# Kernel tuning notes

Hardware: AMD Instinct MI355X
Metric: run time of the kernel (lower is better)

Reference implementation:

```python
import jax, jax.numpy as jnp
import numpy as np

SLOPE = 0.2  # leaky_relu_slope for both LVC block and kernel predictor (passed through)
DILATIONS = (1, 3, 9, 27)
HOP = 256
STRIDE = 8
IN_CH = 32
KSZ = 3  # conv_kernel_size


def conv1d(x, w, b, dilation=1, padding=0):
    # x: (B,C,T), w: (O,I,K) torch layout
    y = jax.lax.conv_general_dilated(
        x, w, window_strides=(1,), padding=[(padding, padding)],
        rhs_dilation=(dilation,), dimension_numbers=('NCH', 'OIH', 'NCH'))
    return y + b[None, :, None]


def conv_transpose1d(x, w, b, stride, padding, output_padding=0):
    # w: torch ConvTranspose1d layout (Cin, Cout, K)
    w_ = jnp.flip(w, -1).transpose(1, 0, 2)  # (Cout, Cin, K)
    K = w.shape[2]
    pad = (K - 1 - padding, K - 1 - padding + output_padding)
    y = jax.lax.conv_general_dilated(
        x, w_, window_strides=(1,), padding=[pad],
        lhs_dilation=(stride,), dimension_numbers=('NCH', 'OIH', 'NCH'))
    return y + b[None, :, None]


def lrelu(x, slope=SLOPE):
    return jnp.where(x >= 0, x, slope * x)


def location_variable_convolution(x, kernel, bias, hop):
    # x: (B,C,T), kernel: (B,C,O,k,L), bias: (B,O,L); T == L*hop; dilation==1 path
    B, C, T = x.shape
    _, _, O, k, L = kernel.shape
    pad = (k - 1) // 2
    xp = jnp.pad(x, ((0, 0), (0, 0), (pad, pad)))
    # gather per-segment sliding windows: (L, hop, k) index into time axis
    idx = (jnp.arange(L)[:, None, None] * hop
           + jnp.arange(hop)[None, :, None]
           + jnp.arange(k)[None, None, :])
    xw = xp[:, :, idx]  # (B, C, L, hop, k)
    o = jnp.einsum('bclsk,bcokl->bols', xw, kernel)  # (B, O, L, hop)
    o = o + bias[:, :, :, None]
    return o.reshape(B, O, L * hop)


def kernel_predictor(spec, kp_in_w, kp_in_b, rb_w1, rb_b1, rb_w2, rb_b2,
                     kern_w, kern_b, bias_w, bias_b):
    B, _, L = spec.shape
    h = conv1d(spec, kp_in_w, kp_in_b, padding=2)  # k=5, pad=2
    for i in range(3):  # num_blocks = 3
        r = h
        h = conv1d(h, rb_w1[i], rb_b1[i], padding=1)
        h = lrelu(h)
        h = conv1d(h, rb_w2[i], rb_b2[i], padding=1)
        h = lrelu(h) + r
    kh = conv1d(h, kern_w, kern_b, padding=1)
    bh = conv1d(h, bias_w, bias_b, padding=1)
    n_layers = len(DILATIONS)
    kernels = kh.reshape(B, n_layers, IN_CH, 2 * IN_CH, KSZ, L)
    biases = bh.reshape(B, n_layers, 2 * IN_CH, L)
    return kernels, biases


def reference(hidden_states, spectrogram, convt_w, convt_b, kp_in_w, kp_in_b,
              rb_w1, rb_b1, rb_w2, rb_b2, kern_w, kern_b, bias_w, bias_b,
              lvc_w, lvc_b):
    h = conv_transpose1d(hidden_states, convt_w, convt_b,
                         stride=STRIDE, padding=STRIDE // 2 + STRIDE % 2,
                         output_padding=STRIDE % 2)
    kernels, biases = kernel_predictor(spectrogram, kp_in_w, kp_in_b,
                                       rb_w1, rb_b1, rb_w2, rb_b2,
                                       kern_w, kern_b, bias_w, bias_b)
    for i, d in enumerate(DILATIONS):
        r = h
        h = lrelu(h)
        h = conv1d(h, lvc_w[i], lvc_b[i], dilation=d, padding=d * (KSZ - 1) // 2)
        h = lrelu(h)
        h = location_variable_convolution(h, kernels[:, i], biases[:, i], HOP)
        h = jax.nn.sigmoid(h[:, :IN_CH, :]) * jnp.tanh(h[:, IN_CH:, :]) + r
    return h


def setup_inputs() -> dict:
    key = jax.random.key(0)
    ks = jax.random.split(key, 12)
    B, COND, L, H = 4, 100, 256, 64
    T = L * HOP  # 65536 output samples
    s = jnp.float32(0.02)
    d = {}
    d['hidden_states'] = jax.random.normal(ks[0], (B, IN_CH, T // STRIDE), jnp.float32)
    d['spectrogram'] = jax.random.normal(ks[1], (B, COND, L), jnp.float32)
    d['convt_w'] = jax.random.normal(ks[2], (IN_CH, IN_CH, 2 * STRIDE), jnp.float32) * s
    d['convt_b'] = jnp.zeros((IN_CH,), jnp.float32)
    d['kp_in_w'] = jax.random.normal(ks[3], (H, COND, 5), jnp.float32) * s
    d['kp_in_b'] = jnp.zeros((H,), jnp.float32)
    d['rb_w1'] = jax.random.normal(ks[4], (3, H, H, 3), jnp.float32) * s
    d['rb_b1'] = jnp.zeros((3, H), jnp.float32)
    d['rb_w2'] = jax.random.normal(ks[5], (3, H, H, 3), jnp.float32) * s
    d['rb_b2'] = jnp.zeros((3, H), jnp.float32)
    KC = IN_CH * 2 * IN_CH * KSZ * len(DILATIONS)  # 24576
    d['kern_w'] = jax.random.normal(ks[6], (KC, H, 3), jnp.float32) * s
    d['kern_b'] = jnp.zeros((KC,), jnp.float32)
    BC = 2 * IN_CH * len(DILATIONS)  # 256
    d['bias_w'] = jax.random.normal(ks[7], (BC, H, 3), jnp.float32) * s
    d['bias_b'] = jnp.zeros((BC,), jnp.float32)
    d['lvc_w'] = jax.random.normal(ks[8], (len(DILATIONS), IN_CH, IN_CH, 3), jnp.float32) * s
    d['lvc_b'] = jnp.zeros((len(DILATIONS), IN_CH), jnp.float32)
    return d
```

## Files before the change

kernel.cpp:

```cpp
#include <hip/hip_runtime.h>
#include <math.h>

#define NB 4
#define T 65536
#define TIN 8192
#define LL 256
#define KCL 6144

__device__ __forceinline__ float lrelu_f(float v) { return v >= 0.f ? v : 0.2f * v; }

__global__ void __launch_bounds__(256, 3) convt_kernel(const float* __restrict__ x,
                                                       const float* __restrict__ w,
                                                       const float* __restrict__ bias,
                                                       float* __restrict__ out) {
    const int bx = blockIdx.x, mt = blockIdx.y, b = blockIdx.z;
    const int tid = threadIdx.x;
    const int lane = tid & 63, wv = tid >> 6;
    const int s0base = bx * 256;
    __shared__ float xs[32][264];
    __shared__ float wm[64][64];

    const float* xb = x + (size_t)b * 32 * TIN;
    for (int idx = tid; idx < 32 * 64; idx += 256) {
        int c = idx >> 6, q = idx & 63;
        int p = s0base + q * 4;
        float4 v = (p + 3 < TIN) ? *(const float4*)(xb + c * TIN + p)
                                 : make_float4(0.f, 0.f, 0.f, 0.f);
        *(float4*)&xs[c][4 + 4 * q] = v;
    }
    if (tid < 32) {
        int p = s0base - 1;
        xs[tid][3] = (p >= 0) ? xb[tid * TIN + p] : 0.f;
    }
    for (int idx = tid; idx < 4096; idx += 256) {
        int i = idx >> 6, mm = idx & 63;
        int oo = mt * 8 + (mm >> 3), k0 = mm & 7;
        wm[i][mm] = (i < 32) ? w[i * 512 + oo * 16 + k0]
                             : w[(i - 32) * 512 + oo * 16 + k0 + 8];
    }
    __syncthreads();

    float acc[2][8][4];
#pragma unroll
    for (int ol = 0; ol < 2; ++ol) {
        float bo = bias[mt * 8 + wv * 2 + ol];
#pragma unroll
        for (int k0 = 0; k0 < 8; ++k0)
#pragma unroll
            for (int si = 0; si < 4; ++si) acc[ol][k0][si] = bo;
    }

    for (int c = 0; c < 32; ++c) {
        float xm1[4], x0[4];
#pragma unroll
        for (int si = 0; si < 4; ++si) {
            xm1[si] = xs[c][lane + si * 64 + 3];
            x0[si]  = xs[c][lane + si * 64 + 4];
        }
        float w0[16], w1[16];
#pragma unroll
        for (int q = 0; q < 4; ++q) {
            *(float4*)&w0[q * 4] = *(const float4*)&wm[c][wv * 16 + q * 4];
            *(float4*)&w1[q * 4] = *(const float4*)&wm[32 + c][wv * 16 + q * 4];
        }
#pragma unroll
        for (int ol = 0; ol < 2; ++ol)
#pragma unroll
            for (int k0 = 0; k0 < 8; ++k0)
#pragma unroll
                for (int si = 0; si < 4; ++si)
                    acc[ol][k0][si] += x0[si] * w0[ol * 8 + k0] + xm1[si] * w1[ol * 8 + k0];
    }

#pragma unroll
    for (int ol = 0; ol < 2; ++ol) {
        float* ob = out + ((size_t)b * 32 + mt * 8 + wv * 2 + ol) * T;
#pragma unroll
        for (int si = 0; si < 4; ++si) {
            int tb = (s0base + lane + si * 64) * 8 - 4;
            if (tb >= 0 && tb < T)
                *(float4*)(ob + tb) = make_float4(acc[ol][0][si], acc[ol][1][si],
                                                  acc[ol][2][si], acc[ol][3][si]);
            if (tb + 4 >= 0 && tb + 4 < T)
                *(float4*)(ob + tb + 4) = make_float4(acc[ol][4][si], acc[ol][5][si],
                                                      acc[ol][6][si], acc[ol][7][si]);
        }
    }
}

__global__ void __launch_bounds__(512) trunk_fused(
    const float* __restrict__ spec,
    const float* __restrict__ kp_in_w, const float* __restrict__ kp_in_b,
    const float* __restrict__ rb_w1, const float* __restrict__ rb_b1,
    const float* __restrict__ rb_w2, const float* __restrict__ rb_b2,
    const float* __restrict__ bias_w, const float* __restrict__ bias_b,
    float* __restrict__ kp_h, float* __restrict__ bh) {
    const int lq = blockIdx.x, b = blockIdx.y;
    const int tid = threadIdx.x;
    const int j = tid & 63;
    const int wvu = tid >> 6;
    const int oc0 = wvu * 8;
    const int l0 = lq * 32;
    const int labs = l0 - 9 + j;
    const bool lvalid = (labs >= 0 && labs < 256);

    __shared__ float hs[64][56];
    __shared__ float xsp[20][56];
    __shared__ float wt[192][68];

    float pw[24];
    float px[3];

    auto pf_kpin = [&](int cc) {
#pragma unroll
        for (int t = 0; t < 13; ++t) {
            int idx = t * 512 + tid;
            pw[t] = 0.f;
            if (idx < 6400) pw[t] = kp_in_w[(size_t)(idx / 100) * 500 + cc * 100 + (idx % 100)];
        }
    };
    auto wr_kpin = [&]() {
#pragma unroll
        for (int t = 0; t < 13; ++t) {
            int idx = t * 512 + tid;
            if (idx < 6400) wt[idx % 100][idx / 100] = pw[t];
        }
    };
    auto pf_xsp = [&](int cc) {
#pragma unroll
        for (int t = 0; t < 3; ++t) {
            int idx = t * 512 + tid;
            px[t] = 0.f;
            if (idx < 1120) {
                int c = idx / 56, jj = idx - c * 56;
                int l = l0 - 9 + jj;
                if (l >= 0 && l < 256)
                    px[t] = spec[((size_t)b * 100 + cc * 20 + c) * LL + l];
            }
        }
    };
    auto wr_xsp = [&]() {
#pragma unroll
        for (int t = 0; t < 3; ++t) {
            int idx = t * 512 + tid;
            if (idx < 1120) xsp[idx / 56][idx % 56] = px[t];
        }
    };
    auto pf_w192 = [&](const float* src) {
#pragma unroll
        for (int t = 0; t < 24; ++t) pw[t] = src[t * 512 + tid];
    };
    auto wr_w192 = [&]() {
#pragma unroll
        for (int t = 0; t < 24; ++t) {
            int idx = t * 512 + tid;
            wt[idx % 192][idx / 192] = pw[t];
        }
    };
    auto conv64 = [&](int jlo, int jhi, const float* bptr, float* a) {
#pragma unroll
        for (int oi = 0; oi < 8; ++oi) a[oi] = bptr[oc0 + oi];
        if (j >= jlo && j < jhi) {
            for (int c = 0; c < 64; ++c) {
                float x0 = hs[c][j - 1], x1 = hs[c][j], x2 = hs[c][j + 1];
#pragma unroll
                for (int k = 0; k < 3; ++k) {
                    float xk = (k == 0) ? x0 : (k == 1) ? x1 : x2;
                    float w8[8];
                    *(float4*)&w8[0] = *(const float4*)&wt[c * 3 + k][oc0];
                    *(float4*)&w8[4] = *(const float4*)&wt[c * 3 + k][oc0 + 4];
#pragma unroll
                    for (int oi = 0; oi < 8; ++oi) a[oi] += xk * w8[oi];
                }
            }
        }
    };

    pf_kpin(0); pf_xsp(0);
    wr_kpin(); wr_xsp();
    __syncthreads();

    float acc[8];
#pragma unroll
    for (int oi = 0; oi < 8; ++oi) acc[oi] = kp_in_b[oc0 + oi];

    for (int cc = 0; cc < 5; ++cc) {
        if (cc < 4) { pf_kpin(cc + 1); pf_xsp(cc + 1); }
        else        { pf_w192(rb_w1); }
        if (j >= 2 && j < 48) {
            for (int c = 0; c < 20; ++c) {
                float x5[5];
#pragma unroll
                for (int u = 0; u < 5; ++u) x5[u] = xsp[c][j - 2 + u];
#pragma unroll
                for (int k = 0; k < 5; ++k) {
                    float w8[8];
                    *(float4*)&w8[0] = *(const float4*)&wt[c * 5 + k][oc0];
                    *(float4*)&w8[4] = *(const float4*)&wt[c * 5 + k][oc0 + 4];
#pragma unroll
                    for (int oi = 0; oi < 8; ++oi) acc[oi] += x5[k] * w8[oi];
                }
            }
        }
        if (cc == 4 && j >= 2 && j < 48) {
#pragma unroll
            for (int oi = 0; oi < 8; ++oi) hs[oc0 + oi][j] = lvalid ? acc[oi] : 0.f;
        }
        __syncthreads();
        if (cc < 4) { wr_kpin(); wr_xsp(); }
        else        { wr_w192(); }
        __syncthreads();
    }

    for (int i = 0; i < 3; ++i) {
        const int jlo1 = 3 + 2 * i, jhi1 = 47 - 2 * i;
        const int jlo2 = jlo1 + 1, jhi2 = jhi1 - 1;
        float r[8];
        if (j >= jlo2 && j < jhi2) {
#pragma unroll
            for (int oi = 0; oi < 8; ++oi) r[oi] = hs[oc0 + oi][j];
        }
        pf_w192(rb_w2 + (size_t)i * 12288);
        float a1[8];
        conv64(jlo1, jhi1, rb_b1 + i * 64, a1);
        __syncthreads();
        if (j >= jlo1 && j < jhi1) {
#pragma unroll
            for (int oi = 0; oi < 8; ++oi) hs[oc0 + oi][j] = lvalid ? lrelu_f(a1[oi]) : 0.f;
        }
        wr_w192();
        __syncthreads();
        pf_w192(i < 2 ? rb_w1 + (size_t)(i + 1) * 12288 : bias_w);
        float a2[8];
        conv64(jlo2, jhi2, rb_b2 + i * 64, a2);
        __syncthreads();
        if (j >= jlo2 && j < jhi2) {
#pragma unroll
            for (int oi = 0; oi < 8; ++oi) hs[oc0 + oi][j] = lvalid ? (lrelu_f(a2[oi]) + r[oi]) : 0.f;
        }
        wr_w192();
        __syncthreads();
    }

    for (int idx = tid; idx < 64 * 32; idx += 512) {
        int c = idx >> 5, jj = idx & 31;
        kp_h[((size_t)b * 64 + c) * LL + l0 + jj] = hs[c][9 + jj];
    }

    for (int g = 0; g < 4; ++g) {
        if (g < 3) pf_w192(bias_w + (size_t)(g + 1) * 12288);
        float a[8];
        conv64(9, 41, bias_b + g * 64, a);
        if (j >= 9 && j < 41) {
#pragma unroll
            for (int oi = 0; oi < 8; ++oi)
                bh[((size_t)b * 256 + g * 64 + oc0 + oi) * LL + labs] = a[oi];
        }
        if (g < 3) {
            __syncthreads();
            wr_w192();
            __syncthreads();
        }
    }
}

__global__ void __launch_bounds__(256, 3) kern_head(const float* __restrict__ kp_h,
                                                    const float* __restrict__ kw,
                                                    const float* __restrict__ kb,
                                                    float* __restrict__ kh, int layer) {
    const int bx = blockIdx.x, b = blockIdx.y;
    const int g = bx >> 1, oc0 = (bx & 1) * 32;
    const int ci = g / 3, kk = g - ci * 3;
    const int tid = threadIdx.x, lane = tid & 63, wv = tid >> 6;
    __shared__ float xs[32][264];
    __shared__ float ws[96][36];

    float acc[8][4];
#pragma unroll
    for (int oi = 0; oi < 8; ++oi) {
        float bv = kb[layer * KCL + (ci * 64 + oc0 + wv * 8 + oi) * 3 + kk];
#pragma unroll
        for (int si = 0; si < 4; ++si) acc[oi][si] = bv;
    }

    const float* wbase = kw + (size_t)layer * KCL * 192;
    for (int half = 0; half < 2; ++half) {
        const int hc0 = half * 32;
        __syncthreads();
        for (int idx = tid; idx < 32 * 64; idx += 256) {
            int c = idx >> 6, q = idx & 63;
            *(float4*)&xs[c][4 + 4 * q] =
                *(const float4*)(kp_h + ((size_t)b * 64 + hc0 + c) * LL + 4 * q);
        }
        if (tid < 32) { xs[tid][3] = 0.f; xs[tid][260] = 0.f; }
        for (int idx = tid; idx < 3072; idx += 256) {
            int ocl = idx / 96, jj = idx - ocl * 96;
            ws[jj][ocl] = wbase[(size_t)((ci * 64 + oc0 + ocl) * 3 + kk) * 192 + hc0 * 3 + jj];
        }
        __syncthreads();
        for (int c = 0; c < 32; ++c) {
#pragma unroll
            for (int t = 0; t < 3; ++t) {
                float wv8[8];
                *(float4*)&wv8[0] = *(const float4*)&ws[c * 3 + t][wv * 8];
                *(float4*)&wv8[4] = *(const float4*)&ws[c * 3 + t][wv * 8 + 4];
                float xv[4];
#pragma unroll
                for (int si = 0; si < 4; ++si) xv[si] = xs[c][lane + si * 64 + t + 3];
#pragma unroll
                for (int oi = 0; oi < 8; ++oi)
#pragma unroll
                    for (int si = 0; si < 4; ++si)
                        acc[oi][si] += wv8[oi] * xv[si];
            }
        }
    }

#pragma unroll
    for (int si = 0; si < 4; ++si) {
        int l = lane + si * 64;
        float* op = kh + ((size_t)b * LL + l) * KCL + g * 64 + oc0 + wv * 8;
        *(float4*)(op)     = make_float4(acc[0][si], acc[1][si], acc[2][si], acc[3][si]);
        *(float4*)(op + 4) = make_float4(acc[4][si], acc[5][si], acc[6][si], acc[7][si]);
    }
}

__global__ void __launch_bounds__(512, 4) layer_fused(
    const float* __restrict__ kh, const float* __restrict__ bh,
    const float* __restrict__ w, const float* __restrict__ bias,
    const float* __restrict__ hin, float* __restrict__ hout,
    int layer, int dil) {
    const int l = blockIdx.x, b = blockIdx.y;
    const int tid = threadIdx.x, lane = tid & 63, wv = tid >> 6;
    const int t0 = l * 256;
    __shared__ float xh[32][316];
    __shared__ float ks[KCL];
    __shared__ float ws[96][36];

    const float* hb = hin + (size_t)b * 32 * T;
    for (int idx = tid; idx < 32 * 316; idx += 512) {
        int c = idx / 316, jj = idx - c * 316;
        int t = t0 + jj - 32;
        xh[c][jj] = (t >= 0 && t < T) ? lrelu_f(hb[(size_t)c * T + t]) : 0.f;
    }
    {
        const float4* kp = (const float4*)(kh + ((size_t)b * LL + l) * KCL);
        float4* kd = (float4*)ks;
        for (int idx = tid; idx < KCL / 4; idx += 512) kd[idx] = kp[idx];
    }
    for (int idx = tid; idx < 3072; idx += 512) {
        int oc = idx / 96, ck = idx - oc * 96;
        ws[ck][oc] = w[oc * 96 + ck];
    }
    __syncthreads();

    const int oc4 = wv * 4;
    float yv[5][4];
    {
        float a[5][4];
#pragma unroll
        for (int oi = 0; oi < 4; ++oi) {
            float bv = bias[oc4 + oi];
#pragma unroll
            for (int si = 0; si < 5; ++si) a[si][oi] = bv;
        }
        for (int c = 0; c < 32; ++c) {
#pragma unroll
            for (int k = 0; k < 3; ++k) {
                float4 wq = *(const float4*)&ws[c * 3 + k][oc4];
                float xv[5];
#pragma unroll
                for (int si = 0; si < 5; ++si) {
                    int col = lane + si * 64;
                    int colc = (col < 258) ? col : 257;
                    xv[si] = xh[c][colc + 31 + (k - 1) * dil];
                }
#pragma unroll
                for (int si = 0; si < 5; ++si) {
                    a[si][0] += xv[si] * wq.x;
                    a[si][1] += xv[si] * wq.y;
                    a[si][2] += xv[si] * wq.z;
                    a[si][3] += xv[si] * wq.w;
                }
            }
        }
#pragma unroll
        for (int si = 0; si < 5; ++si) {
            int t = t0 - 1 + lane + si * 64;
            bool tval = (t >= 0 && t < T);
#pragma unroll
            for (int oi = 0; oi < 4; ++oi)
                yv[si][oi] = tval ? lrelu_f(a[si][oi]) : 0.f;
        }
    }
    __syncthreads();

#pragma unroll
    for (int si = 0; si < 5; ++si) {
        int col = lane + si * 64;
        if (col < 258) {
#pragma unroll
            for (int oi = 0; oi < 4; ++oi) xh[oc4 + oi][col + 31] = yv[si][oi];
        }
    }
    __syncthreads();

    const int oc8 = (wv & 3) * 8;
    const int sh  = wv >> 2;
    float acc_a[8][2], acc_g[8][2];
#pragma unroll
    for (int oi = 0; oi < 8; ++oi) {
        float ba = bh[((size_t)b * 256 + layer * 64 + oc8 + oi) * LL + l];
        float bg = bh[((size_t)b * 256 + layer * 64 + 32 + oc8 + oi) * LL + l];
#pragma unroll
        for (int si = 0; si < 2; ++si) { acc_a[oi][si] = ba; acc_g[oi][si] = bg; }
    }

    for (int c = 0; c < 32; ++c) {
#pragma unroll
        for (int k = 0; k < 3; ++k) {
            const float* kr = ks + (c * 3 + k) * 64;
            float wa[8], wg[8];
            *(float4*)&wa[0] = *(const float4*)(kr + oc8);
            *(float4*)&wa[4] = *(const float4*)(kr + oc8 + 4);
            *(float4*)&wg[0] = *(const float4*)(kr + 32 + oc8);
            *(float4*)&wg[4] = *(const float4*)(kr + 32 + oc8 + 4);
            float xv2[2];
#pragma unroll
            for (int si = 0; si < 2; ++si) {
                int s = lane + (sh * 2 + si) * 64;
                xv2[si] = xh[c][s + k + 31];
            }
#pragma unroll
            for (int oi = 0; oi < 8; ++oi)
#pragma unroll
                for (int si = 0; si < 2; ++si) {
                    acc_a[oi][si] += wa[oi] * xv2[si];
                    acc_g[oi][si] += wg[oi] * xv2[si];
                }
        }
    }

#pragma unroll
    for (int oi = 0; oi < 8; ++oi) {
        const float* hip = hin + ((size_t)b * 32 + oc8 + oi) * T + t0;
        float* hop = hout + ((size_t)b * 32 + oc8 + oi) * T + t0;
#pragma unroll
        for (int si = 0; si < 2; ++si) {
            int s = lane + (sh * 2 + si) * 64;
            float a = acc_a[oi][si], g = acc_g[oi][si];
            float sg = 1.f / (1.f + __expf(-a));
            float th = tanhf(g);
            hop[s] = sg * th + hip[s];
        }
    }
}

extern "C" void kernel_launch(void* const* d_in, const int* in_sizes, int n_in,
                              void* d_out, int out_size, void* d_ws, size_t ws_size,
                              hipStream_t stream) {
    const float* hidden  = (const float*)d_in[0];
    const float* spec    = (const float*)d_in[1];
    const float* convt_w = (const float*)d_in[2];
    const float* convt_b = (const float*)d_in[3];
    const float* kp_in_w = (const float*)d_in[4];
    const float* kp_in_b = (const float*)d_in[5];
    const float* rb_w1   = (const float*)d_in[6];
    const float* rb_b1   = (const float*)d_in[7];
    const float* rb_w2   = (const float*)d_in[8];
    const float* rb_b2   = (const float*)d_in[9];
    const float* kern_w  = (const float*)d_in[10];
    const float* kern_b  = (const float*)d_in[11];
    const float* bias_w  = (const float*)d_in[12];
    const float* bias_b  = (const float*)d_in[13];
    const float* lvc_w   = (const float*)d_in[14];
    const float* lvc_b   = (const float*)d_in[15];

    float* wsp = (float*)d_ws;
    float* h_ws     = wsp;
    float* kh_layer = h_ws + (size_t)NB * 32 * T;
    float* bh       = kh_layer + (size_t)NB * LL * KCL;
    float* kp_h     = bh + (size_t)NB * 256 * LL;

    float* h0 = (float*)d_out;
    float* h1 = h_ws;

    convt_kernel<<<dim3(33, 4, NB), 256, 0, stream>>>(hidden, convt_w, convt_b, h0);

    trunk_fused<<<dim3(8, NB), 512, 0, stream>>>(spec, kp_in_w, kp_in_b,
                                                 rb_w1, rb_b1, rb_w2, rb_b2,
                                                 bias_w, bias_b, kp_h, bh);

    static const int dil[4] = {1, 3, 9, 27};
    float* hin = h0;
    float* hout = h1;
    for (int layer = 0; layer < 4; ++layer) {
        kern_head<<<dim3(192, NB), 256, 0, stream>>>(kp_h, kern_w, kern_b, kh_layer, layer);
        layer_fused<<<dim3(LL, NB), 512, 0, stream>>>(
            kh_layer, bh, lvc_w + (size_t)layer * 32 * 32 * 3, lvc_b + layer * 32,
            hin, hout, layer, dil[layer]);
        float* tmp = hin; hin = hout; hout = tmp;
    }
}
```

Measured before the change: 785.3 us.

## Merge convT and trunk into one launch, move bias head into kern_head

Combines the transposed-conv kernel and the kernel-predictor trunk into a single launch. The two share LDS through a union and split the work by block index, and each convT block now handles 16 output channels with 512 threads. The serial 4-group bias-head convolution leaves the 32-block trunk and runs as 8 extra blocks per batch in the first kern_head launch. The layer_fused halo load also gets a vectorized float4 path for the interior. The aim is to cut launch count and the long serial tail of the small trunk kernel, at the cost of more code complexity and uneven block workloads inside one grid.

```diff
diff --git a/kernel.cpp b/kernel.cpp
--- a/kernel.cpp
+++ b/kernel.cpp
@@ -9,104 +9,113 @@
 
 __device__ __forceinline__ float lrelu_f(float v) { return v >= 0.f ? v : 0.2f * v; }
 
-__global__ void __launch_bounds__(256, 3) convt_kernel(const float* __restrict__ x,
-                                                       const float* __restrict__ w,
-                                                       const float* __restrict__ bias,
-                                                       float* __restrict__ out) {
-    const int bx = blockIdx.x, mt = blockIdx.y, b = blockIdx.z;
-    const int tid = threadIdx.x;
-    const int lane = tid & 63, wv = tid >> 6;
-    const int s0base = bx * 256;
-    __shared__ float xs[32][264];
-    __shared__ float wm[64][64];
-
-    const float* xb = x + (size_t)b * 32 * TIN;
-    for (int idx = tid; idx < 32 * 64; idx += 256) {
-        int c = idx >> 6, q = idx & 63;
-        int p = s0base + q * 4;
-        float4 v = (p + 3 < TIN) ? *(const float4*)(xb + c * TIN + p)
-                                 : make_float4(0.f, 0.f, 0.f, 0.f);
-        *(float4*)&xs[c][4 + 4 * q] = v;
-    }
-    if (tid < 32) {
-        int p = s0base - 1;
-        xs[tid][3] = (p >= 0) ? xb[tid * TIN + p] : 0.f;
-    }
-    for (int idx = tid; idx < 4096; idx += 256) {
-        int i = idx >> 6, mm = idx & 63;
-        int oo = mt * 8 + (mm >> 3), k0 = mm & 7;
-        wm[i][mm] = (i < 32) ? w[i * 512 + oo * 16 + k0]
-                             : w[(i - 32) * 512 + oo * 16 + k0 + 8];
-    }
-    __syncthreads();
-
-    float acc[2][8][4];
-#pragma unroll
-    for (int ol = 0; ol < 2; ++ol) {
-        float bo = bias[mt * 8 + wv * 2 + ol];
-#pragma unroll
-        for (int k0 = 0; k0 < 8; ++k0)
-#pragma unroll
-            for (int si = 0; si < 4; ++si) acc[ol][k0][si] = bo;
-    }
-
-    for (int c = 0; c < 32; ++c) {
-        float xm1[4], x0[4];
-#pragma unroll
-        for (int si = 0; si < 4; ++si) {
-            xm1[si] = xs[c][lane + si * 64 + 3];
-            x0[si]  = xs[c][lane + si * 64 + 4];
-        }
-        float w0[16], w1[16];
-#pragma unroll
-        for (int q = 0; q < 4; ++q) {
-            *(float4*)&w0[q * 4] = *(const float4*)&wm[c][wv * 16 + q * 4];
-            *(float4*)&w1[q * 4] = *(const float4*)&wm[32 + c][wv * 16 + q * 4];
-        }
-#pragma unroll
-        for (int ol = 0; ol < 2; ++ol)
-#pragma unroll
-            for (int k0 = 0; k0 < 8; ++k0)
-#pragma unroll
-                for (int si = 0; si < 4; ++si)
-                    acc[ol][k0][si] += x0[si] * w0[ol * 8 + k0] + xm1[si] * w1[ol * 8 + k0];
-    }
-
-#pragma unroll
-    for (int ol = 0; ol < 2; ++ol) {
-        float* ob = out + ((size_t)b * 32 + mt * 8 + wv * 2 + ol) * T;
-#pragma unroll
-        for (int si = 0; si < 4; ++si) {
-            int tb = (s0base + lane + si * 64) * 8 - 4;
-            if (tb >= 0 && tb < T)
-                *(float4*)(ob + tb) = make_float4(acc[ol][0][si], acc[ol][1][si],
-                                                  acc[ol][2][si], acc[ol][3][si]);
-            if (tb + 4 >= 0 && tb + 4 < T)
-                *(float4*)(ob + tb + 4) = make_float4(acc[ol][4][si], acc[ol][5][si],
-                                                      acc[ol][6][si], acc[ol][7][si]);
-        }
-    }
-}
-
-__global__ void __launch_bounds__(512) trunk_fused(
+union Phase1LDS {
+    struct { float xs[32][264]; float wm[64][128]; } cvt;
+    struct { float hs[64][56]; float xsp[20][56]; float wt[192][68]; } trk;
+};
+
+__global__ void __launch_bounds__(512) phase1(
+    const float* __restrict__ x, const float* __restrict__ cw,
+    const float* __restrict__ cbias, float* __restrict__ hout,
     const float* __restrict__ spec,
     const float* __restrict__ kp_in_w, const float* __restrict__ kp_in_b,
     const float* __restrict__ rb_w1, const float* __restrict__ rb_b1,
     const float* __restrict__ rb_w2, const float* __restrict__ rb_b2,
-    const float* __restrict__ bias_w, const float* __restrict__ bias_b,
-    float* __restrict__ kp_h, float* __restrict__ bh) {
-    const int lq = blockIdx.x, b = blockIdx.y;
+    float* __restrict__ kp_h) {
+    __shared__ Phase1LDS u;
+    const int bid = blockIdx.x;
     const int tid = threadIdx.x;
-    const int j = tid & 63;
-    const int wvu = tid >> 6;
-    const int oc0 = wvu * 8;
+    const int lane = tid & 63, wv = tid >> 6;
+
+    if (bid < 264) {
+        const int bx = bid % 33;
+        const int rr = bid / 33;
+        const int mtp = rr & 1;
+        const int b = rr >> 1;
+        const int s0base = bx * 256;
+        float (*xs)[264] = u.cvt.xs;
+        float (*wm)[128] = u.cvt.wm;
+
+        const float* xb = x + (size_t)b * 32 * TIN;
+        for (int idx = tid; idx < 32 * 64; idx += 512) {
+            int c = idx >> 6, q = idx & 63;
+            int p = s0base + q * 4;
+            float4 v = (p + 3 < TIN) ? *(const float4*)(xb + c * TIN + p)
+                                     : make_float4(0.f, 0.f, 0.f, 0.f);
+            *(float4*)&xs[c][4 + 4 * q] = v;
+        }
+        if (tid < 32) {
+            int p = s0base - 1;
+            xs[tid][3] = (p >= 0) ? xb[tid * TIN + p] : 0.f;
+        }
+        for (int idx = tid; idx < 8192; idx += 512) {
+            int i = idx >> 7, mm = idx & 127;
+            int oo = mtp * 16 + (mm >> 3), k0 = mm & 7;
+            wm[i][mm] = (i < 32) ? cw[i * 512 + oo * 16 + k0]
+                                 : cw[(i - 32) * 512 + oo * 16 + k0 + 8];
+        }
+        __syncthreads();
+
+        float acc[2][8][4];
+#pragma unroll
+        for (int ol = 0; ol < 2; ++ol) {
+            float bo = cbias[mtp * 16 + wv * 2 + ol];
+#pragma unroll
+            for (int k0 = 0; k0 < 8; ++k0)
+#pragma unroll
+                for (int si = 0; si < 4; ++si) acc[ol][k0][si] = bo;
+        }
+
+        for (int c = 0; c < 32; ++c) {
+            float xm1[4], x0[4];
+#pragma unroll
+            for (int si = 0; si < 4; ++si) {
+                xm1[si] = xs[c][lane + si * 64 + 3];
+                x0[si]  = xs[c][lane + si * 64 + 4];
+            }
+            float w0[16], w1[16];
+#pragma unroll
+            for (int q = 0; q < 4; ++q) {
+                *(float4*)&w0[q * 4] = *(const float4*)&wm[c][wv * 16 + q * 4];
+                *(float4*)&w1[q * 4] = *(const float4*)&wm[32 + c][wv * 16 + q * 4];
+            }
+#pragma unroll
+            for (int ol = 0; ol < 2; ++ol)
+#pragma unroll
+                for (int k0 = 0; k0 < 8; ++k0)
+#pragma unroll
+                    for (int si = 0; si < 4; ++si)
+                        acc[ol][k0][si] += x0[si] * w0[ol * 8 + k0] + xm1[si] * w1[ol * 8 + k0];
+        }
+
+#pragma unroll
+        for (int ol = 0; ol < 2; ++ol) {
+            float* ob = hout + ((size_t)b * 32 + mtp * 16 + wv * 2 + ol) * T;
+#pragma unroll
+            for (int si = 0; si < 4; ++si) {
+                int tb = (s0base + lane + si * 64) * 8 - 4;
+                if (tb >= 0 && tb < T)
+                    *(float4*)(ob + tb) = make_float4(acc[ol][0][si], acc[ol][1][si],
+                                                      acc[ol][2][si], acc[ol][3][si]);
+                if (tb + 4 >= 0 && tb + 4 < T)
+                    *(float4*)(ob + tb + 4) = make_float4(acc[ol][4][si], acc[ol][5][si],
+                                                          acc[ol][6][si], acc[ol][7][si]);
+            }
+        }
+        return;
+    }
+
+    const int tb = bid - 264;
+    const int lq = tb & 7, b = tb >> 3;
+    const int j = lane;
+    const int oc0 = wv * 8;
     const int l0 = lq * 32;
     const int labs = l0 - 9 + j;
     const bool lvalid = (labs >= 0 && labs < 256);
 
-    __shared__ float hs[64][56];
-    __shared__ float xsp[20][56];
-    __shared__ float wt[192][68];
+    float (*hs)[56] = u.trk.hs;
+    float (*xsp)[56] = u.trk.xsp;
+    float (*wt)[68] = u.trk.wt;
 
     float pw[24];
     float px[3];
@@ -191,7 +200,7 @@
             for (int c = 0; c < 20; ++c) {
                 float x5[5];
 #pragma unroll
-                for (int u = 0; u < 5; ++u) x5[u] = xsp[c][j - 2 + u];
+                for (int u2 = 0; u2 < 5; ++u2) x5[u2] = xsp[c][j - 2 + u2];
 #pragma unroll
                 for (int k = 0; k < 5; ++k) {
                     float w8[8];
@@ -230,7 +239,7 @@
         }
         wr_w192();
         __syncthreads();
-        pf_w192(i < 2 ? rb_w1 + (size_t)(i + 1) * 12288 : bias_w);
+        if (i < 2) pf_w192(rb_w1 + (size_t)(i + 1) * 12288);
         float a2[8];
         conv64(jlo2, jhi2, rb_b2 + i * 64, a2);
         __syncthreads();
@@ -238,7 +247,7 @@
 #pragma unroll
             for (int oi = 0; oi < 8; ++oi) hs[oc0 + oi][j] = lvalid ? (lrelu_f(a2[oi]) + r[oi]) : 0.f;
         }
-        wr_w192();
+        if (i < 2) wr_w192();
         __syncthreads();
     }
 
@@ -246,44 +255,47 @@
         int c = idx >> 5, jj = idx & 31;
         kp_h[((size_t)b * 64 + c) * LL + l0 + jj] = hs[c][9 + jj];
     }
-
-    for (int g = 0; g < 4; ++g) {
-        if (g < 3) pf_w192(bias_w + (size_t)(g + 1) * 12288);
-        float a[8];
-        conv64(9, 41, bias_b + g * 64, a);
-        if (j >= 9 && j < 41) {
-#pragma unroll
-            for (int oi = 0; oi < 8; ++oi)
-                bh[((size_t)b * 256 + g * 64 + oc0 + oi) * LL + labs] = a[oi];
-        }
-        if (g < 3) {
-            __syncthreads();
-            wr_w192();
-            __syncthreads();
-        }
-    }
 }
 
 __global__ void __launch_bounds__(256, 3) kern_head(const float* __restrict__ kp_h,
                                                     const float* __restrict__ kw,
                                                     const float* __restrict__ kb,
-                                                    float* __restrict__ kh, int layer) {
+                                                    const float* __restrict__ bias_w,
+                                                    const float* __restrict__ bias_b,
+                                                    float* __restrict__ kh,
+                                                    float* __restrict__ bh, int layer) {
     const int bx = blockIdx.x, b = blockIdx.y;
-    const int g = bx >> 1, oc0 = (bx & 1) * 32;
-    const int ci = g / 3, kk = g - ci * 3;
+    const bool isbias = (bx >= 192);
     const int tid = threadIdx.x, lane = tid & 63, wv = tid >> 6;
     __shared__ float xs[32][264];
     __shared__ float ws[96][36];
 
+    int g = 0, oc0 = 0, ci = 0, kk = 0, ocb0 = 0;
+    const float* wsrc;
+    size_t wrow0;
+    int wstride;
+    if (!isbias) {
+        g = bx >> 1; oc0 = (bx & 1) * 32;
+        ci = g / 3; kk = g - ci * 3;
+        wsrc = kw + (size_t)layer * KCL * 192;
+        wrow0 = (size_t)((ci * 64 + oc0) * 3 + kk) * 192;
+        wstride = 576;
+    } else {
+        ocb0 = (bx - 192) * 32;
+        wsrc = bias_w;
+        wrow0 = (size_t)ocb0 * 192;
+        wstride = 192;
+    }
+
     float acc[8][4];
 #pragma unroll
     for (int oi = 0; oi < 8; ++oi) {
-        float bv = kb[layer * KCL + (ci * 64 + oc0 + wv * 8 + oi) * 3 + kk];
+        float bv = isbias ? bias_b[ocb0 + wv * 8 + oi]
+                          : kb[layer * KCL + (ci * 64 + oc0 + wv * 8 + oi) * 3 + kk];
 #pragma unroll
         for (int si = 0; si < 4; ++si) acc[oi][si] = bv;
     }
 
-    const float* wbase = kw + (size_t)layer * KCL * 192;
     for (int half = 0; half < 2; ++half) {
         const int hc0 = half * 32;
         __syncthreads();
@@ -295,7 +307,7 @@
         if (tid < 32) { xs[tid][3] = 0.f; xs[tid][260] = 0.f; }
         for (int idx = tid; idx < 3072; idx += 256) {
             int ocl = idx / 96, jj = idx - ocl * 96;
-            ws[jj][ocl] = wbase[(size_t)((ci * 64 + oc0 + ocl) * 3 + kk) * 192 + hc0 * 3 + jj];
+            ws[jj][ocl] = wsrc[wrow0 + (size_t)ocl * wstride + hc0 * 3 + jj];
         }
         __syncthreads();
         for (int c = 0; c < 32; ++c) {
@@ -316,12 +328,22 @@
         }
     }
 
-#pragma unroll
-    for (int si = 0; si < 4; ++si) {
-        int l = lane + si * 64;
-        float* op = kh + ((size_t)b * LL + l) * KCL + g * 64 + oc0 + wv * 8;
-        *(float4*)(op)     = make_float4(acc[0][si], acc[1][si], acc[2][si], acc[3][si]);
-        *(float4*)(op + 4) = make_float4(acc[4][si], acc[5][si], acc[6][si], acc[7][si]);
+    if (!isbias) {
+#pragma unroll
+        for (int si = 0; si < 4; ++si) {
+            int l = lane + si * 64;
+            float* op = kh + ((size_t)b * LL + l) * KCL + g * 64 + oc0 + wv * 8;
+            *(float4*)(op)     = make_float4(acc[0][si], acc[1][si], acc[2][si], acc[3][si]);
+            *(float4*)(op + 4) = make_float4(acc[4][si], acc[5][si], acc[6][si], acc[7][si]);
+        }
+    } else {
+#pragma unroll
+        for (int oi = 0; oi < 8; ++oi) {
+            float* op = bh + ((size_t)b * 256 + ocb0 + wv * 8 + oi) * LL;
+#pragma unroll
+            for (int si = 0; si < 4; ++si)
+                op[lane + si * 64] = acc[oi][si];
+        }
     }
 }
 
@@ -338,8 +360,15 @@
     __shared__ float ws[96][36];
 
     const float* hb = hin + (size_t)b * 32 * T;
-    for (int idx = tid; idx < 32 * 316; idx += 512) {
-        int c = idx / 316, jj = idx - c * 316;
+    for (int idx = tid; idx < 32 * 64; idx += 512) {
+        int c = idx >> 6, q = idx & 63;
+        float4 v = *(const float4*)(hb + (size_t)c * T + t0 + 4 * q);
+        *(float4*)&xh[c][32 + 4 * q] = make_float4(lrelu_f(v.x), lrelu_f(v.y),
+                                                   lrelu_f(v.z), lrelu_f(v.w));
+    }
+    for (int idx = tid; idx < 32 * 60; idx += 512) {
+        int c = idx / 60, r = idx - c * 60;
+        int jj = (r < 32) ? r : (256 + r);
         int t = t0 + jj - 32;
         xh[c][jj] = (t >= 0 && t < T) ? lrelu_f(hb[(size_t)c * T + t]) : 0.f;
     }
@@ -485,17 +514,16 @@
     float* h0 = (float*)d_out;
     float* h1 = h_ws;
 
-    convt_kernel<<<dim3(33, 4, NB), 256, 0, stream>>>(hidden, convt_w, convt_b, h0);
-
-    trunk_fused<<<dim3(8, NB), 512, 0, stream>>>(spec, kp_in_w, kp_in_b,
-                                                 rb_w1, rb_b1, rb_w2, rb_b2,
-                                                 bias_w, bias_b, kp_h, bh);
+    phase1<<<dim3(296), 512, 0, stream>>>(hidden, convt_w, convt_b, h0,
+                                          spec, kp_in_w, kp_in_b,
+                                          rb_w1, rb_b1, rb_w2, rb_b2, kp_h);
 
     static const int dil[4] = {1, 3, 9, 27};
     float* hin = h0;
     float* hout = h1;
     for (int layer = 0; layer < 4; ++layer) {
-        kern_head<<<dim3(192, NB), 256, 0, stream>>>(kp_h, kern_w, kern_b, kh_layer, layer);
+        kern_head<<<dim3(layer == 0 ? 200 : 192, NB), 256, 0, stream>>>(
+            kp_h, kern_w, kern_b, bias_w, bias_b, kh_layer, bh, layer);
         layer_fused<<<dim3(LL, NB), 512, 0, stream>>>(
             kh_layer, bh, lvc_w + (size_t)layer * 32 * 32 * 3, lvc_b + layer * 32,
             hin, hout, layer, dil[layer]);
```

Measured after the change: 723.7 us. -7.9%, faster.
